# Kernel optimization log

Hardware: AMD Instinct MI355X
Metric: run time of the kernel (lower is better)

Reference implementation:

```python
import jax, jax.numpy as jnp
import numpy as np

N = 50000      # num nodes
E = 800000     # num edges (avg degree 16)
IN_FEA = 256
OU_FEA = 64


def setup_inputs() -> dict:
    key = jax.random.key(0)
    k_h, k_w, k_r, k_c, k_v = jax.random.split(key, 5)
    h = jax.random.normal(k_h, (N, IN_FEA), dtype=jnp.float32)
    # Linear(in_fea, ou_fea, bias=None): weight applied as h @ W, W [IN, OUT]
    W = jax.random.normal(k_w, (IN_FEA, OU_FEA), dtype=jnp.float32) / np.sqrt(IN_FEA)
    row = jax.random.randint(k_r, (E,), 0, N, dtype=jnp.int32)
    col = jax.random.randint(k_c, (E,), 0, N, dtype=jnp.int32)
    vals = jax.random.uniform(k_v, (E,), dtype=jnp.float32)
    return {"h": h, "W": W, "row": row, "col": col, "vals": vals}


def reference(h, W, row, col, vals):
    # dense projection: [N, IN] @ [IN, OUT] -> [N, OUT]
    hp = h @ W
    # torch builds sparse tensor with indices [col, row], i.e. G = A^T,
    # so torch.sparse.mm(G, hp)[i] = sum over edges with col==i of vals * hp[row]
    msg = hp[row] * vals[:, None]                      # [E, OUT] gather + scale
    out = jax.ops.segment_sum(msg, col, num_segments=N)  # scatter-add to dest
    return out
```

## Files before the change

### kernel.cpp

```cpp
#include <hip/hip_runtime.h>
#include <hip/hip_bf16.h>

#define IN_F 256
#define OU_F 64
#define BKN 128
#define BSHIFT 7
#define CHUNK 1024
#define STAGE_CAP 4096

typedef __attribute__((ext_vector_type(8))) short short8;
typedef __attribute__((ext_vector_type(4))) float f32x4;

__global__ void __launch_bounds__(256)
gemm_mfma_kernel(const float* __restrict__ h, const float* __restrict__ W,
                 __hip_bfloat16* __restrict__ hp, int N)
{
    __shared__ unsigned short Wt[64][264];
    __shared__ uint4 hsv[2048];
    unsigned char* hs = reinterpret_cast<unsigned char*>(hsv);
    const int t = threadIdx.x;

#pragma unroll
    for (int i = 0; i < 32; ++i) {
        int p  = t + i * 256;
        int c  = p & 63;
        int k0 = (p >> 6) << 1;
        float x = W[(size_t)k0 * OU_F + c];
        float y = W[(size_t)(k0 + 1) * OU_F + c];
        __hip_bfloat162 bb = __float22bfloat162_rn(make_float2(x, y));
        *reinterpret_cast<unsigned*>(&Wt[c][k0]) = *reinterpret_cast<unsigned*>(&bb);
    }

    const int rbase = blockIdx.x * 64;
    const int nrow  = min(64, N - rbase);
#pragma unroll
    for (int i = 0; i < 16; ++i) {
        int idx = t + i * 256;
        int r  = idx >> 6;
        int k4 = idx & 63;
        float4 v = make_float4(0.f, 0.f, 0.f, 0.f);
        if (r < nrow)
            v = reinterpret_cast<const float4*>(h)[(size_t)(rbase + r) * (IN_F / 4) + k4];
        __hip_bfloat162 lo = __float22bfloat162_rn(make_float2(v.x, v.y));
        __hip_bfloat162 hi = __float22bfloat162_rn(make_float2(v.z, v.w));
        unsigned boff = (unsigned)r * 512u + (((unsigned)k4 * 8u) ^ (((unsigned)r & 7u) << 4));
        uint2 pk;
        pk.x = *reinterpret_cast<unsigned*>(&lo);
        pk.y = *reinterpret_cast<unsigned*>(&hi);
        *reinterpret_cast<uint2*>(&hs[boff]) = pk;
    }
    __syncthreads();

    const int l    = t & 63;
    const int wv   = t >> 6;
    const int cl   = l & 15;
    const int kg   = l >> 4;
    const int rloc = wv * 16 + cl;

    f32x4 acc[4];
#pragma unroll
    for (int nt = 0; nt < 4; ++nt) acc[nt] = (f32x4){0.f, 0.f, 0.f, 0.f};

#pragma unroll
    for (int ks = 0; ks < 8; ++ks) {
        unsigned aoff = (unsigned)rloc * 512u +
                        (((unsigned)(ks * 64 + kg * 16)) ^ (((unsigned)rloc & 7u) << 4));
        short8 af = *reinterpret_cast<const short8*>(&hs[aoff]);
#pragma unroll
        for (int nt = 0; nt < 4; ++nt) {
            short8 bf = *reinterpret_cast<const short8*>(&Wt[nt * 16 + cl][ks * 32 + kg * 8]);
            acc[nt] = __builtin_amdgcn_mfma_f32_16x16x32_bf16(af, bf, acc[nt], 0, 0, 0);
        }
    }

#pragma unroll
    for (int nt = 0; nt < 4; ++nt)
#pragma unroll
        for (int rg = 0; rg < 4; ++rg) {
            int rr = rbase + wv * 16 + kg * 4 + rg;
            if (rr < N)
                hp[(size_t)rr * OU_F + nt * 16 + cl] = __float2bfloat16(acc[nt][rg]);
        }
}

__global__ void __launch_bounds__(256)
hist_kernel(const int* __restrict__ col, int* __restrict__ bcnt, int E, int NB)
{
    __shared__ int lh[512];
    const int t = threadIdx.x;
    lh[t] = 0; lh[t + 256] = 0;
    __syncthreads();
    const int n4 = E >> 2;
    const int4* c4 = (const int4*)col;
    for (int i = blockIdx.x * 256 + t; i < n4; i += gridDim.x * 256) {
        int4 v = c4[i];
        atomicAdd(&lh[v.x >> BSHIFT], 1);
        atomicAdd(&lh[v.y >> BSHIFT], 1);
        atomicAdd(&lh[v.z >> BSHIFT], 1);
        atomicAdd(&lh[v.w >> BSHIFT], 1);
    }
    if (blockIdx.x == 0)
        for (int e = (n4 << 2) + t; e < E; e += 256)
            atomicAdd(&lh[col[e] >> BSHIFT], 1);
    __syncthreads();
    for (int i = t; i < NB; i += 256)
        if (lh[i]) atomicAdd(&bcnt[i], lh[i]);
}

__global__ void __launch_bounds__(256)
scan_kernel(const int* __restrict__ bcnt, int* __restrict__ boffs,
            int* __restrict__ bcursor, int NB)
{
    __shared__ int c[512];
    __shared__ int s[256];
    const int t = threadIdx.x;
    c[t]       = (t < NB)       ? bcnt[t] : 0;
    c[t + 256] = (t + 256 < NB) ? bcnt[t + 256] : 0;
    __syncthreads();
    s[t] = c[2 * t] + c[2 * t + 1];
    __syncthreads();
    for (int d = 1; d < 256; d <<= 1) {
        int v = (t >= d) ? s[t - d] : 0;
        __syncthreads();
        s[t] += v;
        __syncthreads();
    }
    int excl = (t > 0) ? s[t - 1] : 0;
    int e0 = excl;
    int e1 = excl + c[2 * t];
    if (2 * t < NB)     { boffs[2 * t]     = e0; bcursor[2 * t]     = e0; }
    if (2 * t + 1 < NB) { boffs[2 * t + 1] = e1; bcursor[2 * t + 1] = e1; }
    if (t == 255) boffs[NB] = s[255];
}

__global__ void __launch_bounds__(256)
partition_kernel(const int* __restrict__ row, const int* __restrict__ col,
                 const float* __restrict__ vals, int* __restrict__ bcursor,
                 int2* __restrict__ epk, int E, int NB)
{
    __shared__ int  hist[512];
    __shared__ int  X[512];
    __shared__ int  gshift[512];
    __shared__ int  s[256];
    __shared__ int2 stage[CHUNK];
    __shared__ int  gpos[CHUNK];

    const int t = threadIdx.x;
    const int base = blockIdx.x * CHUNK;
    const int n = min(CHUNK, E - base);

    hist[t] = 0; hist[t + 256] = 0;
    __syncthreads();

#pragma unroll
    for (int k = 0; k < CHUNK / 256; ++k) {
        int i = t + k * 256;
        if (i < n) atomicAdd(&hist[col[base + i] >> BSHIFT], 1);
    }
    __syncthreads();

    s[t] = hist[2 * t] + hist[2 * t + 1];
    __syncthreads();
    for (int d = 1; d < 256; d <<= 1) {
        int v = (t >= d) ? s[t - d] : 0;
        __syncthreads();
        s[t] += v;
        __syncthreads();
    }
    int excl = (t > 0) ? s[t - 1] : 0;
    X[2 * t]     = excl;
    X[2 * t + 1] = excl + hist[2 * t];
    __syncthreads();

    for (int i = t; i < NB; i += 256) {
        int hcnt = hist[i];
        int g = hcnt ? atomicAdd(&bcursor[i], hcnt) : 0;
        gshift[i] = g - X[i];
    }
    __syncthreads();

#pragma unroll
    for (int k = 0; k < CHUNK / 256; ++k) {
        int i = t + k * 256;
        if (i < n) {
            int e  = base + i;
            int cv = col[e];
            int b  = cv >> BSHIFT;
            int r  = atomicAdd(&X[b], 1);
            unsigned pk = (unsigned)row[e] | ((unsigned)(cv & (BKN - 1)) << 17);
            stage[r] = make_int2((int)pk, __float_as_int(vals[e]));
            gpos[r]  = gshift[b] + r;
        }
    }
    __syncthreads();

#pragma unroll
    for (int k = 0; k < CHUNK / 256; ++k) {
        int i = t + k * 256;
        if (i < n) epk[gpos[i]] = stage[i];
    }
}

__global__ void __launch_bounds__(256)
csr_kernel(const int2* __restrict__ epk, const int* __restrict__ boffs,
           int2* __restrict__ epk2, int* __restrict__ node_offs,
           int N, int NB)
{
    __shared__ int  cnt[BKN];
    __shared__ int  sc[BKN];
    __shared__ int  cur[BKN];
    __shared__ int2 stage[STAGE_CAP];
    const int t = threadIdx.x;
    const int b = blockIdx.x;
    const int s = boffs[b], e = boffs[b + 1];
    const int n = e - s;
    const int node0 = b << BSHIFT;

    if (t < BKN) cnt[t] = 0;
    __syncthreads();
    for (int i = t; i < n; i += 256)
        atomicAdd(&cnt[((unsigned)epk[s + i].x) >> 17], 1);
    __syncthreads();

    if (t < BKN) sc[t] = cnt[t];
    __syncthreads();
    for (int d = 1; d < BKN; d <<= 1) {
        int v = 0;
        if (t < BKN && t >= d) v = sc[t - d];
        __syncthreads();
        if (t < BKN) sc[t] += v;
        __syncthreads();
    }
    if (t < BKN) {
        int excl = sc[t] - cnt[t];
        cur[t] = excl;
        int node = node0 + t;
        if (node < N) node_offs[node] = s + excl;
    }
    if (b == NB - 1 && t == 0) node_offs[N] = e;
    __syncthreads();

    if (n <= STAGE_CAP) {
        for (int i = t; i < n; i += 256) {
            int2 r = epk[s + i];
            int pos = atomicAdd(&cur[((unsigned)r.x) >> 17], 1);
            stage[pos] = r;
        }
        __syncthreads();
        for (int i = t; i < n; i += 256)
            epk2[s + i] = stage[i];
    } else {
        for (int i = t; i < n; i += 256) {
            int2 r = epk[s + i];
            int pos = atomicAdd(&cur[((unsigned)r.x) >> 17], 1);
            epk2[s + pos] = r;
        }
    }
}

__global__ void __launch_bounds__(256)
gather_kernel(const __hip_bfloat16* __restrict__ hp, const int* __restrict__ node_offs,
              const int2* __restrict__ epk2, float* __restrict__ out, int N)
{
    int wid  = (int)((blockIdx.x * 256u + threadIdx.x) >> 6);
    int lane = threadIdx.x & 63;
    if (wid >= N) return;
    int s = node_offs[wid], e = node_offs[wid + 1];
    float acc = 0.f;
    for (int base = s; base < e; base += 64) {
        int n = min(64, e - base);
        int2 m = make_int2(0, 0);
        if (lane < n) m = epk2[base + lane];
        int j = 0;
        for (; j + 4 <= n; j += 4) {
            unsigned r0 = (unsigned)__shfl(m.x, j)     & 0x1FFFFu;
            unsigned r1 = (unsigned)__shfl(m.x, j + 1) & 0x1FFFFu;
            unsigned r2 = (unsigned)__shfl(m.x, j + 2) & 0x1FFFFu;
            unsigned r3 = (unsigned)__shfl(m.x, j + 3) & 0x1FFFFu;
            float v0 = __int_as_float(__shfl(m.y, j));
            float v1 = __int_as_float(__shfl(m.y, j + 1));
            float v2 = __int_as_float(__shfl(m.y, j + 2));
            float v3 = __int_as_float(__shfl(m.y, j + 3));
            float x0 = __bfloat162float(hp[((size_t)r0 << 6) + lane]);
            float x1 = __bfloat162float(hp[((size_t)r1 << 6) + lane]);
            float x2 = __bfloat162float(hp[((size_t)r2 << 6) + lane]);
            float x3 = __bfloat162float(hp[((size_t)r3 << 6) + lane]);
            acc = fmaf(v0, x0, acc);
            acc = fmaf(v1, x1, acc);
            acc = fmaf(v2, x2, acc);
            acc = fmaf(v3, x3, acc);
        }
        for (; j < n; ++j) {
            unsigned r = (unsigned)__shfl(m.x, j) & 0x1FFFFu;
            float    v = __int_as_float(__shfl(m.y, j));
            acc = fmaf(v, __bfloat162float(hp[((size_t)r << 6) + lane]), acc);
        }
    }
    out[(size_t)wid * OU_F + lane] = acc;
}

__global__ void __launch_bounds__(256)
scatter_kernel(const __hip_bfloat16* __restrict__ hp, const int* __restrict__ row,
               const int* __restrict__ col, const float* __restrict__ vals,
               float* __restrict__ out, int E)
{
    unsigned int gid = blockIdx.x * 256u + threadIdx.x;
    int e = (int)(gid >> 6);
    if (e >= E) return;
    int f = (int)(gid & 63u);
    int r = row[e], c = col[e];
    float m = vals[e] * __bfloat162float(hp[(size_t)r * OU_F + f]);
    __hip_atomic_fetch_add(&out[(size_t)c * OU_F + f], m,
                           __ATOMIC_RELAXED, __HIP_MEMORY_SCOPE_AGENT);
}

extern "C" void kernel_launch(void* const* d_in, const int* in_sizes, int n_in,
                              void* d_out, int out_size, void* d_ws, size_t ws_size,
                              hipStream_t stream)
{
    const float* h    = (const float*)d_in[0];
    const float* W    = (const float*)d_in[1];
    const int*   row  = (const int*)d_in[2];
    const int*   col  = (const int*)d_in[3];
    const float* vals = (const float*)d_in[4];
    float*       out  = (float*)d_out;

    const int N = in_sizes[0] / IN_F;
    const int E = in_sizes[2];
    const int NB = (N + BKN - 1) / BKN;

    char*  ws  = (char*)d_ws;
    size_t off = 0;
    auto alloc = [&](size_t bytes) -> char* {
        char* p = ws + off;
        off = (off + bytes + 255) & ~(size_t)255;
        return p;
    };
    __hip_bfloat16* hp = (__hip_bfloat16*)alloc((size_t)N * OU_F * 2);
    int*   bcnt      = (int*)  alloc((size_t)NB * 4);
    int*   boffs     = (int*)  alloc((size_t)(NB + 1) * 4);
    int*   bcursor   = (int*)  alloc((size_t)NB * 4);
    int*   node_offs = (int*)  alloc((size_t)(N + 1) * 4);
    int2*  epk       = (int2*) alloc((size_t)E * 8);
    int2*  epk2      = (int2*) alloc((size_t)E * 8);
    const bool fits = (off <= ws_size) && (NB <= 512) && (N < 131072);

    const int ntiles = (N + 63) / 64;
    gemm_mfma_kernel<<<ntiles, 256, 0, stream>>>(h, W, hp, N);

    if (fits) {
        hipMemsetAsync(bcnt, 0, (size_t)NB * 4, stream);
        hist_kernel<<<256, 256, 0, stream>>>(col, bcnt, E, NB);
        scan_kernel<<<1, 256, 0, stream>>>(bcnt, boffs, bcursor, NB);
        partition_kernel<<<(E + CHUNK - 1) / CHUNK, 256, 0, stream>>>(
            row, col, vals, bcursor, epk, E, NB);
        csr_kernel<<<NB, 256, 0, stream>>>(epk, boffs, epk2, node_offs, N, NB);
        gather_kernel<<<(N + 3) / 4, 256, 0, stream>>>(hp, node_offs, epk2, out, N);
    } else {
        hipMemsetAsync(d_out, 0, (size_t)out_size * sizeof(float), stream);
        unsigned long long total = (unsigned long long)E * 64ull;
        unsigned int sgrid = (unsigned int)((total + 255ull) / 256ull);
        scatter_kernel<<<sgrid, 256, 0, stream>>>(hp, row, col, vals, out, E);
    }
}
```

Before: 97.51 us.

## Fuse CSR build with gather, merge hist and scan, drop memset

Halves the bucket size to 64 nodes and fuses the per-bucket CSR sort with the gather. Each block sorts its bucket's edges into shared memory and then reduces them directly, so the epk2/node_offs round trip through global memory goes away. The histogram and scan are merged through a last-block-done pattern, and the bcnt zeroing moves into the GEMM kernel, which removes a memset and a launch. Partition now uses larger 4096-edge chunks with a 1024-bucket histogram. Risks include lower occupancy from the larger shared arrays and load imbalance, with only 4 waves per 64-node block doing the gather.

```diff
diff --git a/kernel.cpp b/kernel.cpp
--- a/kernel.cpp
+++ b/kernel.cpp
@@ -3,22 +3,26 @@
 
 #define IN_F 256
 #define OU_F 64
-#define BKN 128
-#define BSHIFT 7
-#define CHUNK 1024
-#define STAGE_CAP 4096
+#define BKN 64
+#define BSHIFT 6
+#define NBMAX 1024
+#define CHUNK 4096
+#define CAP 4096
 
 typedef __attribute__((ext_vector_type(8))) short short8;
 typedef __attribute__((ext_vector_type(4))) float f32x4;
 
 __global__ void __launch_bounds__(256)
 gemm_mfma_kernel(const float* __restrict__ h, const float* __restrict__ W,
-                 __hip_bfloat16* __restrict__ hp, int N)
+                 __hip_bfloat16* __restrict__ hp, int* __restrict__ bcnt, int N)
 {
     __shared__ unsigned short Wt[64][264];
     __shared__ uint4 hsv[2048];
     unsigned char* hs = reinterpret_cast<unsigned char*>(hsv);
     const int t = threadIdx.x;
+
+    if (blockIdx.x == 0)
+        for (int i = t; i <= NBMAX; i += 256) bcnt[i] = 0;
 
 #pragma unroll
     for (int i = 0; i < 32; ++i) {
@@ -84,12 +88,17 @@
 }
 
 __global__ void __launch_bounds__(256)
-hist_kernel(const int* __restrict__ col, int* __restrict__ bcnt, int E, int NB)
-{
-    __shared__ int lh[512];
+hist_scan_kernel(const int* __restrict__ col, int* __restrict__ bcnt,
+                 int* __restrict__ boffs, int* __restrict__ bcursor, int E, int NB)
+{
+    __shared__ int lh[NBMAX];
+    __shared__ int s[256];
+    __shared__ int isLast;
     const int t = threadIdx.x;
-    lh[t] = 0; lh[t + 256] = 0;
-    __syncthreads();
+
+    for (int i = t; i < NB; i += 256) lh[i] = 0;
+    __syncthreads();
+
     const int n4 = E >> 2;
     const int4* c4 = (const int4*)col;
     for (int i = blockIdx.x * 256 + t; i < n4; i += gridDim.x * 256) {
@@ -103,21 +112,29 @@
         for (int e = (n4 << 2) + t; e < E; e += 256)
             atomicAdd(&lh[col[e] >> BSHIFT], 1);
     __syncthreads();
+
     for (int i = t; i < NB; i += 256)
         if (lh[i]) atomicAdd(&bcnt[i], lh[i]);
-}
-
-__global__ void __launch_bounds__(256)
-scan_kernel(const int* __restrict__ bcnt, int* __restrict__ boffs,
-            int* __restrict__ bcursor, int NB)
-{
-    __shared__ int c[512];
-    __shared__ int s[256];
-    const int t = threadIdx.x;
-    c[t]       = (t < NB)       ? bcnt[t] : 0;
-    c[t + 256] = (t + 256 < NB) ? bcnt[t + 256] : 0;
-    __syncthreads();
-    s[t] = c[2 * t] + c[2 * t + 1];
+
+    __threadfence();
+    if (t == 0) {
+        int v = atomicAdd(&bcnt[NBMAX], 1);
+        isLast = (v == (int)gridDim.x - 1);
+    }
+    __syncthreads();
+    if (!isLast) return;
+
+    for (int i = t; i < NB; i += 256)
+        lh[i] = __hip_atomic_load(&bcnt[i], __ATOMIC_RELAXED, __HIP_MEMORY_SCOPE_AGENT);
+    __syncthreads();
+
+    int idx = t * 4;
+    int c0 = (idx     < NB) ? lh[idx]     : 0;
+    int c1 = (idx + 1 < NB) ? lh[idx + 1] : 0;
+    int c2 = (idx + 2 < NB) ? lh[idx + 2] : 0;
+    int c3 = (idx + 3 < NB) ? lh[idx + 3] : 0;
+    int s0 = c0, s1 = s0 + c1, s2 = s1 + c2, s3 = s2 + c3;
+    s[t] = s3;
     __syncthreads();
     for (int d = 1; d < 256; d <<= 1) {
         int v = (t >= d) ? s[t - d] : 0;
@@ -126,10 +143,10 @@
         __syncthreads();
     }
     int excl = (t > 0) ? s[t - 1] : 0;
-    int e0 = excl;
-    int e1 = excl + c[2 * t];
-    if (2 * t < NB)     { boffs[2 * t]     = e0; bcursor[2 * t]     = e0; }
-    if (2 * t + 1 < NB) { boffs[2 * t + 1] = e1; bcursor[2 * t + 1] = e1; }
+    if (idx     < NB) { boffs[idx]     = excl;      bcursor[idx]     = excl;      }
+    if (idx + 1 < NB) { boffs[idx + 1] = excl + s0; bcursor[idx + 1] = excl + s0; }
+    if (idx + 2 < NB) { boffs[idx + 2] = excl + s1; bcursor[idx + 2] = excl + s1; }
+    if (idx + 3 < NB) { boffs[idx + 3] = excl + s2; bcursor[idx + 3] = excl + s2; }
     if (t == 255) boffs[NB] = s[255];
 }
 
@@ -138,9 +155,9 @@
                  const float* __restrict__ vals, int* __restrict__ bcursor,
                  int2* __restrict__ epk, int E, int NB)
 {
-    __shared__ int  hist[512];
-    __shared__ int  X[512];
-    __shared__ int  gshift[512];
+    __shared__ int  hist[NBMAX];
+    __shared__ int  X[NBMAX];
+    __shared__ int  gshift[NBMAX];
     __shared__ int  s[256];
     __shared__ int2 stage[CHUNK];
     __shared__ int  gpos[CHUNK];
@@ -149,7 +166,7 @@
     const int base = blockIdx.x * CHUNK;
     const int n = min(CHUNK, E - base);
 
-    hist[t] = 0; hist[t + 256] = 0;
+    for (int i = t; i < NBMAX; i += 256) hist[i] = 0;
     __syncthreads();
 
 #pragma unroll
@@ -159,7 +176,10 @@
     }
     __syncthreads();
 
-    s[t] = hist[2 * t] + hist[2 * t + 1];
+    int idx = t * 4;
+    int c0 = hist[idx], c1 = hist[idx + 1], c2 = hist[idx + 2], c3 = hist[idx + 3];
+    int s0 = c0, s1 = s0 + c1, s2 = s1 + c2, s3 = s2 + c3;
+    s[t] = s3;
     __syncthreads();
     for (int d = 1; d < 256; d <<= 1) {
         int v = (t >= d) ? s[t - d] : 0;
@@ -168,8 +188,10 @@
         __syncthreads();
     }
     int excl = (t > 0) ? s[t - 1] : 0;
-    X[2 * t]     = excl;
-    X[2 * t + 1] = excl + hist[2 * t];
+    X[idx]     = excl;
+    X[idx + 1] = excl + s0;
+    X[idx + 2] = excl + s1;
+    X[idx + 3] = excl + s2;
     __syncthreads();
 
     for (int i = t; i < NB; i += 256) {
@@ -202,101 +224,84 @@
 }
 
 __global__ void __launch_bounds__(256)
-csr_kernel(const int2* __restrict__ epk, const int* __restrict__ boffs,
-           int2* __restrict__ epk2, int* __restrict__ node_offs,
-           int N, int NB)
+csr_gather_kernel(const __hip_bfloat16* __restrict__ hp, const int* __restrict__ boffs,
+                  const int2* __restrict__ epk, float* __restrict__ out, int N)
 {
     __shared__ int  cnt[BKN];
-    __shared__ int  sc[BKN];
     __shared__ int  cur[BKN];
-    __shared__ int2 stage[STAGE_CAP];
+    __shared__ int  noff[BKN + 1];
+    __shared__ int2 stage[CAP];
     const int t = threadIdx.x;
     const int b = blockIdx.x;
     const int s = boffs[b], e = boffs[b + 1];
     const int n = e - s;
     const int node0 = b << BSHIFT;
-
-    if (t < BKN) cnt[t] = 0;
-    __syncthreads();
-    for (int i = t; i < n; i += 256)
-        atomicAdd(&cnt[((unsigned)epk[s + i].x) >> 17], 1);
-    __syncthreads();
-
-    if (t < BKN) sc[t] = cnt[t];
-    __syncthreads();
-    for (int d = 1; d < BKN; d <<= 1) {
-        int v = 0;
-        if (t < BKN && t >= d) v = sc[t - d];
-        __syncthreads();
-        if (t < BKN) sc[t] += v;
-        __syncthreads();
-    }
-    if (t < BKN) {
-        int excl = sc[t] - cnt[t];
-        cur[t] = excl;
-        int node = node0 + t;
-        if (node < N) node_offs[node] = s + excl;
-    }
-    if (b == NB - 1 && t == 0) node_offs[N] = e;
-    __syncthreads();
-
-    if (n <= STAGE_CAP) {
+    const int lane = t & 63;
+    const int wv   = t >> 6;
+
+    if (n <= CAP) {
+        if (t < BKN) cnt[t] = 0;
+        __syncthreads();
+        for (int i = t; i < n; i += 256)
+            atomicAdd(&cnt[((unsigned)epk[s + i].x) >> 17], 1);
+        __syncthreads();
+        if (t < 64) {
+            int v = cnt[t], orig = v;
+            for (int d = 1; d < 64; d <<= 1) {
+                int u = __shfl_up(v, d);
+                if (t >= d) v += u;
+            }
+            noff[t] = v - orig;
+            cur[t]  = v - orig;
+            if (t == 63) noff[64] = v;
+        }
+        __syncthreads();
         for (int i = t; i < n; i += 256) {
             int2 r = epk[s + i];
             int pos = atomicAdd(&cur[((unsigned)r.x) >> 17], 1);
             stage[pos] = r;
         }
         __syncthreads();
-        for (int i = t; i < n; i += 256)
-            epk2[s + i] = stage[i];
+
+        for (int nd = wv; nd < BKN; nd += 4) {
+            int node = node0 + nd;
+            if (node >= N) break;
+            int js = noff[nd], je = noff[nd + 1];
+            float acc = 0.f;
+            int j = js;
+            for (; j + 4 <= je; j += 4) {
+                int2 r0 = stage[j],     r1 = stage[j + 1];
+                int2 r2 = stage[j + 2], r3 = stage[j + 3];
+                float x0 = __bfloat162float(hp[((size_t)(r0.x & 0x1FFFF) << 6) + lane]);
+                float x1 = __bfloat162float(hp[((size_t)(r1.x & 0x1FFFF) << 6) + lane]);
+                float x2 = __bfloat162float(hp[((size_t)(r2.x & 0x1FFFF) << 6) + lane]);
+                float x3 = __bfloat162float(hp[((size_t)(r3.x & 0x1FFFF) << 6) + lane]);
+                acc = fmaf(__int_as_float(r0.y), x0, acc);
+                acc = fmaf(__int_as_float(r1.y), x1, acc);
+                acc = fmaf(__int_as_float(r2.y), x2, acc);
+                acc = fmaf(__int_as_float(r3.y), x3, acc);
+            }
+            for (; j < je; ++j) {
+                int2 r = stage[j];
+                acc = fmaf(__int_as_float(r.y),
+                           __bfloat162float(hp[((size_t)(r.x & 0x1FFFF) << 6) + lane]), acc);
+            }
+            out[(size_t)node * OU_F + lane] = acc;
+        }
     } else {
-        for (int i = t; i < n; i += 256) {
-            int2 r = epk[s + i];
-            int pos = atomicAdd(&cur[((unsigned)r.x) >> 17], 1);
-            epk2[s + pos] = r;
-        }
-    }
-}
-
-__global__ void __launch_bounds__(256)
-gather_kernel(const __hip_bfloat16* __restrict__ hp, const int* __restrict__ node_offs,
-              const int2* __restrict__ epk2, float* __restrict__ out, int N)
-{
-    int wid  = (int)((blockIdx.x * 256u + threadIdx.x) >> 6);
-    int lane = threadIdx.x & 63;
-    if (wid >= N) return;
-    int s = node_offs[wid], e = node_offs[wid + 1];
-    float acc = 0.f;
-    for (int base = s; base < e; base += 64) {
-        int n = min(64, e - base);
-        int2 m = make_int2(0, 0);
-        if (lane < n) m = epk2[base + lane];
-        int j = 0;
-        for (; j + 4 <= n; j += 4) {
-            unsigned r0 = (unsigned)__shfl(m.x, j)     & 0x1FFFFu;
-            unsigned r1 = (unsigned)__shfl(m.x, j + 1) & 0x1FFFFu;
-            unsigned r2 = (unsigned)__shfl(m.x, j + 2) & 0x1FFFFu;
-            unsigned r3 = (unsigned)__shfl(m.x, j + 3) & 0x1FFFFu;
-            float v0 = __int_as_float(__shfl(m.y, j));
-            float v1 = __int_as_float(__shfl(m.y, j + 1));
-            float v2 = __int_as_float(__shfl(m.y, j + 2));
-            float v3 = __int_as_float(__shfl(m.y, j + 3));
-            float x0 = __bfloat162float(hp[((size_t)r0 << 6) + lane]);
-            float x1 = __bfloat162float(hp[((size_t)r1 << 6) + lane]);
-            float x2 = __bfloat162float(hp[((size_t)r2 << 6) + lane]);
-            float x3 = __bfloat162float(hp[((size_t)r3 << 6) + lane]);
-            acc = fmaf(v0, x0, acc);
-            acc = fmaf(v1, x1, acc);
-            acc = fmaf(v2, x2, acc);
-            acc = fmaf(v3, x3, acc);
-        }
-        for (; j < n; ++j) {
-            unsigned r = (unsigned)__shfl(m.x, j) & 0x1FFFFu;
-            float    v = __int_as_float(__shfl(m.y, j));
-            acc = fmaf(v, __bfloat162float(hp[((size_t)r << 6) + lane]), acc);
-        }
-    }
-    out[(size_t)wid * OU_F + lane] = acc;
+        for (int nd = wv; nd < BKN; nd += 4) {
+            int node = node0 + nd;
+            if (node >= N) break;
+            float acc = 0.f;
+            for (int j = s; j < e; ++j) {
+                int2 r = epk[j];
+                if ((int)(((unsigned)r.x) >> 17) == nd)
+                    acc = fmaf(__int_as_float(r.y),
+                               __bfloat162float(hp[((size_t)(r.x & 0x1FFFF) << 6) + lane]), acc);
+            }
+            out[(size_t)node * OU_F + lane] = acc;
+        }
+    }
 }
 
 __global__ void __launch_bounds__(256)
@@ -337,25 +342,20 @@
         return p;
     };
     __hip_bfloat16* hp = (__hip_bfloat16*)alloc((size_t)N * OU_F * 2);
-    int*   bcnt      = (int*)  alloc((size_t)NB * 4);
-    int*   boffs     = (int*)  alloc((size_t)(NB + 1) * 4);
-    int*   bcursor   = (int*)  alloc((size_t)NB * 4);
-    int*   node_offs = (int*)  alloc((size_t)(N + 1) * 4);
-    int2*  epk       = (int2*) alloc((size_t)E * 8);
-    int2*  epk2      = (int2*) alloc((size_t)E * 8);
-    const bool fits = (off <= ws_size) && (NB <= 512) && (N < 131072);
+    int*   bcnt    = (int*)  alloc((size_t)(NBMAX + 1) * 4);
+    int*   boffs   = (int*)  alloc((size_t)(NBMAX + 1) * 4);
+    int*   bcursor = (int*)  alloc((size_t)NBMAX * 4);
+    int2*  epk     = (int2*) alloc((size_t)E * 8);
+    const bool fits = (off <= ws_size) && (NB <= NBMAX) && (N < 131072);
 
     const int ntiles = (N + 63) / 64;
-    gemm_mfma_kernel<<<ntiles, 256, 0, stream>>>(h, W, hp, N);
+    gemm_mfma_kernel<<<ntiles, 256, 0, stream>>>(h, W, hp, bcnt, N);
 
     if (fits) {
-        hipMemsetAsync(bcnt, 0, (size_t)NB * 4, stream);
-        hist_kernel<<<256, 256, 0, stream>>>(col, bcnt, E, NB);
-        scan_kernel<<<1, 256, 0, stream>>>(bcnt, boffs, bcursor, NB);
+        hist_scan_kernel<<<256, 256, 0, stream>>>(col, bcnt, boffs, bcursor, E, NB);
         partition_kernel<<<(E + CHUNK - 1) / CHUNK, 256, 0, stream>>>(
             row, col, vals, bcursor, epk, E, NB);
-        csr_kernel<<<NB, 256, 0, stream>>>(epk, boffs, epk2, node_offs, N, NB);
-        gather_kernel<<<(N + 3) / 4, 256, 0, stream>>>(hp, node_offs, epk2, out, N);
+        csr_gather_kernel<<<NB, 256, 0, stream>>>(hp, boffs, epk, out, N);
     } else {
         hipMemsetAsync(d_out, 0, (size_t)out_size * sizeof(float), stream);
         unsigned long long total = (unsigned long long)E * 64ull;
```

Result: slower. 106.8 us (+9.5%).

## Fuse histogram and scan via last-block pattern, drop memset, enlarge partition chunk

Applied to the files above, without the earlier changes.

Zeroing of the bucket counters moves into block 0 of the GEMM kernel, replacing the separate memset. The histogram and scan kernels merge into one: each block publishes its counts, and the last block to finish, found with an atomic ticket counter, runs the prefix scan. This removes two launches and their dependency gaps. The partition chunk grows from 1024 to 4096 edges per block, which means fewer global cursor atomics but fewer blocks and more shared memory per block, so occupancy may drop.

```diff
diff --git a/kernel.cpp b/kernel.cpp
--- a/kernel.cpp
+++ b/kernel.cpp
@@ -5,7 +5,8 @@
 #define OU_F 64
 #define BKN 128
 #define BSHIFT 7
-#define CHUNK 1024
+#define NBMAX 512
+#define CHUNK 4096
 #define STAGE_CAP 4096
 
 typedef __attribute__((ext_vector_type(8))) short short8;
@@ -13,12 +14,15 @@
 
 __global__ void __launch_bounds__(256)
 gemm_mfma_kernel(const float* __restrict__ h, const float* __restrict__ W,
-                 __hip_bfloat16* __restrict__ hp, int N)
+                 __hip_bfloat16* __restrict__ hp, int* __restrict__ bcnt, int N)
 {
     __shared__ unsigned short Wt[64][264];
     __shared__ uint4 hsv[2048];
     unsigned char* hs = reinterpret_cast<unsigned char*>(hsv);
     const int t = threadIdx.x;
+
+    if (blockIdx.x == 0)
+        for (int i = t; i <= NBMAX; i += 256) bcnt[i] = 0;
 
 #pragma unroll
     for (int i = 0; i < 32; ++i) {
@@ -84,12 +88,17 @@
 }
 
 __global__ void __launch_bounds__(256)
-hist_kernel(const int* __restrict__ col, int* __restrict__ bcnt, int E, int NB)
-{
-    __shared__ int lh[512];
+hist_scan_kernel(const int* __restrict__ col, int* __restrict__ bcnt,
+                 int* __restrict__ boffs, int* __restrict__ bcursor, int E, int NB)
+{
+    __shared__ int lh[NBMAX];
+    __shared__ int s[256];
+    __shared__ int isLast;
     const int t = threadIdx.x;
-    lh[t] = 0; lh[t + 256] = 0;
-    __syncthreads();
+
+    for (int i = t; i < NB; i += 256) lh[i] = 0;
+    __syncthreads();
+
     const int n4 = E >> 2;
     const int4* c4 = (const int4*)col;
     for (int i = blockIdx.x * 256 + t; i < n4; i += gridDim.x * 256) {
@@ -103,21 +112,27 @@
         for (int e = (n4 << 2) + t; e < E; e += 256)
             atomicAdd(&lh[col[e] >> BSHIFT], 1);
     __syncthreads();
+
     for (int i = t; i < NB; i += 256)
         if (lh[i]) atomicAdd(&bcnt[i], lh[i]);
-}
-
-__global__ void __launch_bounds__(256)
-scan_kernel(const int* __restrict__ bcnt, int* __restrict__ boffs,
-            int* __restrict__ bcursor, int NB)
-{
-    __shared__ int c[512];
-    __shared__ int s[256];
-    const int t = threadIdx.x;
-    c[t]       = (t < NB)       ? bcnt[t] : 0;
-    c[t + 256] = (t + 256 < NB) ? bcnt[t + 256] : 0;
-    __syncthreads();
-    s[t] = c[2 * t] + c[2 * t + 1];
+
+    __threadfence();
+    if (t == 0) {
+        int v = atomicAdd(&bcnt[NBMAX], 1);
+        isLast = (v == (int)gridDim.x - 1);
+    }
+    __syncthreads();
+    if (!isLast) return;
+
+    for (int i = t; i < NB; i += 256)
+        lh[i] = __hip_atomic_load(&bcnt[i], __ATOMIC_RELAXED, __HIP_MEMORY_SCOPE_AGENT);
+    __syncthreads();
+
+    int idx = t * 2;
+    int c0 = (idx     < NB) ? lh[idx]     : 0;
+    int c1 = (idx + 1 < NB) ? lh[idx + 1] : 0;
+    int s0 = c0, s1 = s0 + c1;
+    s[t] = s1;
     __syncthreads();
     for (int d = 1; d < 256; d <<= 1) {
         int v = (t >= d) ? s[t - d] : 0;
@@ -126,10 +141,8 @@
         __syncthreads();
     }
     int excl = (t > 0) ? s[t - 1] : 0;
-    int e0 = excl;
-    int e1 = excl + c[2 * t];
-    if (2 * t < NB)     { boffs[2 * t]     = e0; bcursor[2 * t]     = e0; }
-    if (2 * t + 1 < NB) { boffs[2 * t + 1] = e1; bcursor[2 * t + 1] = e1; }
+    if (idx     < NB) { boffs[idx]     = excl;      bcursor[idx]     = excl;      }
+    if (idx + 1 < NB) { boffs[idx + 1] = excl + s0; bcursor[idx + 1] = excl + s0; }
     if (t == 255) boffs[NB] = s[255];
 }
 
@@ -138,9 +151,9 @@
                  const float* __restrict__ vals, int* __restrict__ bcursor,
                  int2* __restrict__ epk, int E, int NB)
 {
-    __shared__ int  hist[512];
-    __shared__ int  X[512];
-    __shared__ int  gshift[512];
+    __shared__ int  hist[NBMAX];
+    __shared__ int  X[NBMAX];
+    __shared__ int  gshift[NBMAX];
     __shared__ int  s[256];
     __shared__ int2 stage[CHUNK];
     __shared__ int  gpos[CHUNK];
@@ -149,7 +162,7 @@
     const int base = blockIdx.x * CHUNK;
     const int n = min(CHUNK, E - base);
 
-    hist[t] = 0; hist[t + 256] = 0;
+    for (int i = t; i < NBMAX; i += 256) hist[i] = 0;
     __syncthreads();
 
 #pragma unroll
@@ -159,7 +172,10 @@
     }
     __syncthreads();
 
-    s[t] = hist[2 * t] + hist[2 * t + 1];
+    int idx = t * 2;
+    int c0 = hist[idx], c1 = hist[idx + 1];
+    int s0 = c0, s1 = s0 + c1;
+    s[t] = s1;
     __syncthreads();
     for (int d = 1; d < 256; d <<= 1) {
         int v = (t >= d) ? s[t - d] : 0;
@@ -168,8 +184,8 @@
         __syncthreads();
     }
     int excl = (t > 0) ? s[t - 1] : 0;
-    X[2 * t]     = excl;
-    X[2 * t + 1] = excl + hist[2 * t];
+    X[idx]     = excl;
+    X[idx + 1] = excl + s0;
     __syncthreads();
 
     for (int i = t; i < NB; i += 256) {
@@ -337,21 +353,19 @@
         return p;
     };
     __hip_bfloat16* hp = (__hip_bfloat16*)alloc((size_t)N * OU_F * 2);
-    int*   bcnt      = (int*)  alloc((size_t)NB * 4);
-    int*   boffs     = (int*)  alloc((size_t)(NB + 1) * 4);
-    int*   bcursor   = (int*)  alloc((size_t)NB * 4);
+    int*   bcnt      = (int*)  alloc((size_t)(NBMAX + 1) * 4);
+    int*   boffs     = (int*)  alloc((size_t)(NBMAX + 1) * 4);
+    int*   bcursor   = (int*)  alloc((size_t)NBMAX * 4);
     int*   node_offs = (int*)  alloc((size_t)(N + 1) * 4);
     int2*  epk       = (int2*) alloc((size_t)E * 8);
     int2*  epk2      = (int2*) alloc((size_t)E * 8);
-    const bool fits = (off <= ws_size) && (NB <= 512) && (N < 131072);
+    const bool fits = (off <= ws_size) && (NB <= NBMAX) && (N < 131072);
 
     const int ntiles = (N + 63) / 64;
-    gemm_mfma_kernel<<<ntiles, 256, 0, stream>>>(h, W, hp, N);
+    gemm_mfma_kernel<<<ntiles, 256, 0, stream>>>(h, W, hp, bcnt, N);
 
     if (fits) {
-        hipMemsetAsync(bcnt, 0, (size_t)NB * 4, stream);
-        hist_kernel<<<256, 256, 0, stream>>>(col, bcnt, E, NB);
-        scan_kernel<<<1, 256, 0, stream>>>(bcnt, boffs, bcursor, NB);
+        hist_scan_kernel<<<256, 256, 0, stream>>>(col, bcnt, boffs, bcursor, E, NB);
         partition_kernel<<<(E + CHUNK - 1) / CHUNK, 256, 0, stream>>>(
             row, col, vals, bcursor, epk, E, NB);
         csr_kernel<<<NB, 256, 0, stream>>>(epk, boffs, epk2, node_offs, N, NB);
```

New measurement: 95.52 us. 2.0% less time.
